# Kernel tuning notes

Hardware: AMD Instinct MI355X
Metric: run time of the kernel (lower is better)

Reference implementation:

```python
import jax, jax.numpy as jnp
import numpy as np

B, DIM, N, K, NA = 1, 64, 1024, 16, 12
POS_HID = 64
ATTN_HID = 4 * DIM


def setup_inputs() -> dict:
    key = jax.random.key(0)
    ks = jax.random.split(key, 8)
    s = 0.05  # small init scale, mimics xavier magnitude
    return {
        "xyz": jax.random.normal(ks[0], (B, 3, N), jnp.float32),
        "feats": jax.random.normal(ks[1], (B, DIM, N, NA), jnp.float32),
        "anchors": jax.random.normal(ks[2], (NA, 3, 3), jnp.float32),
        "to_qkv": jax.random.normal(ks[3], (3 * DIM, DIM), jnp.float32) * s,
        "pos_mlp1": jax.random.normal(ks[4], (POS_HID, 3), jnp.float32) * s,
        "pos_mlp2": jax.random.normal(ks[5], (DIM, POS_HID), jnp.float32) * s,
        "attn_mlp1": jax.random.normal(ks[6], (ATTN_HID, DIM), jnp.float32) * s,
        "attn_mlp2": jax.random.normal(ks[7], (DIM, ATTN_HID), jnp.float32) * s,
    }


def reference(xyz, feats, anchors, to_qkv, pos_mlp1, pos_mlp2, attn_mlp1, attn_mlp2):
    # --- KNN over points (self included) ---
    pts = jnp.swapaxes(xyz, 1, 2)                      # [B,N,3]
    sq = jnp.sum(pts * pts, axis=-1)                   # [B,N]
    d2 = sq[:, :, None] + sq[:, None, :] - 2.0 * jnp.einsum('bnd,bmd->bnm', pts, pts)
    _, idx = jax.lax.top_k(-d2, K)                     # [B,N,K] nearest indices

    # --- gather helpers (vmapped over batch) ---
    gather3 = jax.vmap(lambda x, i: x[:, i])           # [C,N],[N,K] -> [C,N,K]
    gather4 = jax.vmap(lambda x, i: x[:, i, :])        # [C,N,A],[N,K] -> [C,N,K,A]

    # --- relative positions rotated by anchors ---
    grouped_xyz = gather3(xyz, idx)                    # [B,3,N,K]
    rel = xyz[:, :, :, None] - grouped_xyz             # [B,3,N,K]
    gx = jnp.einsum('aij,bjnk->binka', anchors, rel)   # [B,3,N,K,NA]

    # --- positional embedding MLP ---
    pe = jnp.einsum('ji,binka->bjnka', pos_mlp1, gx)   # [B,POS_HID,N,K,NA]
    pe = jax.nn.relu(pe)
    pe = jnp.einsum('ji,binka->bjnka', pos_mlp2, pe)   # [B,DIM,N,K,NA]

    # --- qkv projection ---
    qkv = jnp.einsum('ji,bina->bjna', to_qkv, feats)   # [B,3*DIM,N,NA]
    q, k, v = jnp.split(qkv, 3, axis=1)                # each [B,DIM,N,NA]

    k_g = gather4(k, idx)                              # [B,DIM,N,K,NA]
    v_g = gather4(v, idx) + pe                         # [B,DIM,N,K,NA]
    qk_rel = q[:, :, :, None, :] - k_g                 # [B,DIM,N,K,NA]

    # --- attention MLP on (qk_rel + pe) ---
    sim = qk_rel + pe
    sim = jnp.einsum('ji,binka->bjnka', attn_mlp1, sim)  # [B,4*DIM,N,K,NA]
    sim = jax.nn.relu(sim)
    sim = jnp.einsum('ji,binka->bjnka', attn_mlp2, sim)  # [B,DIM,N,K,NA]

    # --- per-channel softmax over neighbor axis, aggregate ---
    attn = jax.nn.softmax(sim, axis=-2)
    return jnp.sum(attn * v_g, axis=-2)                # [B,DIM,N,NA]
```

## Files before the change

kernel.cpp:

```cpp
#include <hip/hip_runtime.h>

#define NPTS 1024
#define DIM 64
#define KNN 16
#define NA 12
#define NCOL 192
#define XPAD 76

typedef __attribute__((ext_vector_type(8))) short bf16x8;
typedef __attribute__((ext_vector_type(4))) float f32x4;

static __device__ inline unsigned short f2bfu(float x) {
    __bf16 b = (__bf16)x;
    return __builtin_bit_cast(unsigned short, b);
}
static __device__ inline bf16x8 load8_cvt(const float* p) {
    f32x4 u = *(const f32x4*)p;
    f32x4 v = *(const f32x4*)(p + 4);
    bf16x8 r;
    r[0] = (short)f2bfu(u[0]); r[1] = (short)f2bfu(u[1]); r[2] = (short)f2bfu(u[2]); r[3] = (short)f2bfu(u[3]);
    r[4] = (short)f2bfu(v[0]); r[5] = (short)f2bfu(v[1]); r[6] = (short)f2bfu(v[2]); r[7] = (short)f2bfu(v[3]);
    return r;
}

__global__ __launch_bounds__(256) void prep_kernel(const float* __restrict__ feats,
                                                   const float* __restrict__ to_qkv,
                                                   float* __restrict__ qkvT,
                                                   unsigned short* __restrict__ pack,
                                                   const float* __restrict__ pos2,
                                                   const float* __restrict__ am1,
                                                   const float* __restrict__ am2,
                                                   const float* __restrict__ xyz,
                                                   int* __restrict__ idxout) {
    __shared__ unsigned short XT[48][72];
    __shared__ float px[NPTS], py[NPTS], pz[NPTS];
    const int t = threadIdx.x;
    const int n0 = blockIdx.x * 48;

    if (blockIdx.x < 72 && t < 64) {
        int s = blockIdx.x;
        int c16p = t & 15, gp = t >> 4;
        const float* src;
        if (s < 8) {
            int nt = s >> 1, kt = s & 1;
            src = pos2 + (nt * 16 + c16p) * 64 + kt * 32 + gp * 8;
        } else if (s < 40) {
            int u = s - 8, hq = u >> 3, nt = (u >> 1) & 3, kt = u & 1;
            src = am1 + (hq * 64 + nt * 16 + c16p) * 64 + kt * 32 + gp * 8;
        } else {
            int u = s - 40, hq = u >> 3, nt = (u >> 1) & 3, kt = u & 1;
            src = am2 + (nt * 16 + c16p) * 256 + hq * 64 + kt * 32 + gp * 8;
        }
        unsigned short* dst = pack + (s * 64 + t) * 8;
        #pragma unroll
        for (int e = 0; e < 8; ++e) dst[e] = f2bfu(src[e]);
    }

    for (int m = t; m < NPTS; m += 256) {
        px[m] = xyz[m];
        py[m] = xyz[NPTS + m];
        pz[m] = xyz[2 * NPTS + m];
    }
    for (int e = t; e < 48 * 64; e += 256) {
        int c = e % 48, i = e / 48;
        XT[c][i] = f2bfu(feats[i * (NPTS * NA) + n0 + c]);
    }
    __syncthreads();

    const int lane = t & 63, w = t >> 6, c16 = lane & 15, g = lane >> 4;

    {
        bf16x8 bfr[3][2];
        #pragma unroll
        for (int ni = 0; ni < 3; ++ni)
            #pragma unroll
            for (int kt = 0; kt < 2; ++kt) {
                int cd = (w * 3 + ni) * 16 + c16;
                bfr[ni][kt] = load8_cvt(to_qkv + cd * 64 + kt * 32 + g * 8);
            }
        const f32x4 zero4 = {0.f, 0.f, 0.f, 0.f};
        #pragma unroll
        for (int mt = 0; mt < 3; ++mt) {
            f32x4 acc[3] = {zero4, zero4, zero4};
            #pragma unroll
            for (int kt = 0; kt < 2; ++kt) {
                bf16x8 af = *(const bf16x8*)&XT[mt * 16 + c16][kt * 32 + g * 8];
                #pragma unroll
                for (int ni = 0; ni < 3; ++ni)
                    acc[ni] = __builtin_amdgcn_mfma_f32_16x16x32_bf16(af, bfr[ni][kt], acc[ni], 0, 0, 0);
            }
            #pragma unroll
            for (int ni = 0; ni < 3; ++ni) {
                int cd = (w * 3 + ni) * 16 + c16;
                int c = cd >> 6, d = cd & 63;
                #pragma unroll
                for (int r = 0; r < 4; ++r) {
                    int na = n0 + mt * 16 + 4 * g + r;
                    qkvT[c * (NPTS * NA * DIM) + na * 64 + d] = acc[ni][r];
                }
            }
        }
    }

    {
        const int n = blockIdx.x * 4 + w;
        const float xn = px[n], yn = py[n], zn = pz[n];
        const float sqn = xn * xn + yn * yn + zn * zn;
        float dd[16]; int id[16];
        #pragma unroll
        for (int j = 0; j < 16; ++j) {
            int m = j * 64 + lane;
            float xm = px[m], ym = py[m], zm = pz[m];
            float sqm = xm * xm + ym * ym + zm * zm;
            float dot = xn * xm + yn * ym + zn * zm;
            dd[j] = sqn + sqm - 2.f * dot;
            id[j] = m;
        }
        for (int r = 0; r < KNN; ++r) {
            float bd = 1e30f; int bi = 0x7fffffff;
            #pragma unroll
            for (int j = 0; j < 16; ++j)
                if (dd[j] < bd || (dd[j] == bd && id[j] < bi)) { bd = dd[j]; bi = id[j]; }
            #pragma unroll
            for (int mask = 1; mask < 64; mask <<= 1) {
                float od = __shfl_xor(bd, mask);
                int oi = __shfl_xor(bi, mask);
                if (od < bd || (od == bd && oi < bi)) { bd = od; bi = oi; }
            }
            if (lane == 0) idxout[n * KNN + r] = bi;
            #pragma unroll
            for (int j = 0; j < 16; ++j)
                if (id[j] == bi) dd[j] = 1e30f;
        }
    }
}

__global__ __launch_bounds__(512, 4) void attn_main(const float* __restrict__ xyz,
                                                    const float* __restrict__ anchors,
                                                    const float* __restrict__ pos1,
                                                    const unsigned short* __restrict__ pack,
                                                    const float* __restrict__ qT,
                                                    const float* __restrict__ kT,
                                                    const float* __restrict__ vT,
                                                    const int* __restrict__ nn,
                                                    float* __restrict__ out) {
    __shared__ __align__(16) unsigned short XbT[NCOL][XPAD];
    __shared__ __align__(16) unsigned short HqT[NCOL][XPAD];
    __shared__ float relb[KNN][3];
    __shared__ float ab[108];
    __shared__ float gbuf[3][NCOL];
    __shared__ int nidx[KNN];

    const int n = blockIdx.x, t = threadIdx.x;
    const int lane = t & 63, wave = t >> 6;
    const int c16 = lane & 15, g = lane >> 4;
    const int mw = wave & 3;
    const int nw = wave >> 2;

    if (t < 108) ab[t] = anchors[t];
    if (t < KNN) {
        int m = nn[n * KNN + t];
        nidx[t] = m;
        relb[t][0] = xyz[n] - xyz[m];
        relb[t][1] = xyz[NPTS + n] - xyz[NPTS + m];
        relb[t][2] = xyz[2 * NPTS + n] - xyz[2 * NPTS + m];
    }
    __syncthreads();

    for (int e = t; e < 3 * NCOL; e += 512) {
        int row = e / NCOL, col = e % NCOL;
        int a = col >> 4, k = col & 15;
        gbuf[row][col] = ab[a * 9 + row * 3 + 0] * relb[k][0]
                       + ab[a * 9 + row * 3 + 1] * relb[k][1]
                       + ab[a * 9 + row * 3 + 2] * relb[k][2];
    }
    __syncthreads();

    {
        const float p10 = pos1[lane * 3 + 0], p11 = pos1[lane * 3 + 1], p12 = pos1[lane * 3 + 2];
        #pragma unroll
        for (int j = 0; j < 24; ++j) {
            int col = wave + 8 * j;
            float p = p10 * gbuf[0][col] + p11 * gbuf[1][col] + p12 * gbuf[2][col];
            XbT[col][lane] = f2bfu(p > 0.f ? p : 0.f);
        }
    }
    __syncthreads();

    const bf16x8* pk16 = (const bf16x8*)pack;
    const f32x4 zero4 = {0.f, 0.f, 0.f, 0.f};

    f32x4 peacc[6] = {zero4, zero4, zero4, zero4, zero4, zero4};
    #pragma unroll
    for (int kt = 0; kt < 2; ++kt) {
        bf16x8 b0 = pk16[((2 * nw + 0) * 2 + kt) * 64 + lane];
        bf16x8 b1 = pk16[((2 * nw + 1) * 2 + kt) * 64 + lane];
        #pragma unroll
        for (int mi = 0; mi < 3; ++mi) {
            bf16x8 af = *(const bf16x8*)&XbT[(mw + 4 * mi) * 16 + c16][kt * 32 + g * 8];
            peacc[mi * 2 + 0] = __builtin_amdgcn_mfma_f32_16x16x32_bf16(af, b0, peacc[mi * 2 + 0], 0, 0, 0);
            peacc[mi * 2 + 1] = __builtin_amdgcn_mfma_f32_16x16x32_bf16(af, b1, peacc[mi * 2 + 1], 0, 0, 0);
        }
    }

    float vgk[6][4], xreg[6][4];
    {
        const int m0 = nidx[4 * g + 0], m1 = nidx[4 * g + 1];
        const int m2 = nidx[4 * g + 2], m3 = nidx[4 * g + 3];
        #pragma unroll
        for (int mi = 0; mi < 3; ++mi) {
            int a = mw + 4 * mi;
            #pragma unroll
            for (int ni = 0; ni < 2; ++ni) {
                int tile = mi * 2 + ni;
                int d = (2 * nw + ni) * 16 + c16;
                float qv = qT[(n * NA + a) * DIM + d];
                int b0 = (m0 * NA + a) * DIM + d, b1 = (m1 * NA + a) * DIM + d;
                int b2 = (m2 * NA + a) * DIM + d, b3 = (m3 * NA + a) * DIM + d;
                xreg[tile][0] = qv - kT[b0] + peacc[tile][0]; vgk[tile][0] = vT[b0] + peacc[tile][0];
                xreg[tile][1] = qv - kT[b1] + peacc[tile][1]; vgk[tile][1] = vT[b1] + peacc[tile][1];
                xreg[tile][2] = qv - kT[b2] + peacc[tile][2]; vgk[tile][2] = vT[b2] + peacc[tile][2];
                xreg[tile][3] = qv - kT[b3] + peacc[tile][3]; vgk[tile][3] = vT[b3] + peacc[tile][3];
            }
        }
    }
    __syncthreads();
    #pragma unroll
    for (int mi = 0; mi < 3; ++mi)
        #pragma unroll
        for (int ni = 0; ni < 2; ++ni) {
            int tile = mi * 2 + ni;
            int col = (2 * nw + ni) * 16 + c16;
            #pragma unroll
            for (int r = 0; r < 4; ++r)
                XbT[(mw + 4 * mi) * 16 + 4 * g + r][col] = f2bfu(xreg[tile][r]);
        }
    __syncthreads();

    f32x4 sacc[6] = {zero4, zero4, zero4, zero4, zero4, zero4};
    for (int hq = 0; hq < 4; ++hq) {
        f32x4 hacc[6] = {zero4, zero4, zero4, zero4, zero4, zero4};
        #pragma unroll
        for (int kt = 0; kt < 2; ++kt) {
            bf16x8 b0 = pk16[(8 + (hq * 4 + 2 * nw + 0) * 2 + kt) * 64 + lane];
            bf16x8 b1 = pk16[(8 + (hq * 4 + 2 * nw + 1) * 2 + kt) * 64 + lane];
            #pragma unroll
            for (int mi = 0; mi < 3; ++mi) {
                bf16x8 af = *(const bf16x8*)&XbT[(mw + 4 * mi) * 16 + c16][kt * 32 + g * 8];
                hacc[mi * 2 + 0] = __builtin_amdgcn_mfma_f32_16x16x32_bf16(af, b0, hacc[mi * 2 + 0], 0, 0, 0);
                hacc[mi * 2 + 1] = __builtin_amdgcn_mfma_f32_16x16x32_bf16(af, b1, hacc[mi * 2 + 1], 0, 0, 0);
            }
        }
        #pragma unroll
        for (int mi = 0; mi < 3; ++mi)
            #pragma unroll
            for (int ni = 0; ni < 2; ++ni) {
                int tile = mi * 2 + ni;
                int col = (2 * nw + ni) * 16 + c16;
                #pragma unroll
                for (int r = 0; r < 4; ++r)
                    HqT[(mw + 4 * mi) * 16 + 4 * g + r][col] = f2bfu(fmaxf(hacc[tile][r], 0.f));
            }
        __syncthreads();
        #pragma unroll
        for (int kt = 0; kt < 2; ++kt) {
            bf16x8 b0 = pk16[(40 + hq * 8 + (2 * nw + 0) * 2 + kt) * 64 + lane];
            bf16x8 b1 = pk16[(40 + hq * 8 + (2 * nw + 1) * 2 + kt) * 64 + lane];
            #pragma unroll
            for (int mi = 0; mi < 3; ++mi) {
                bf16x8 af = *(const bf16x8*)&HqT[(mw + 4 * mi) * 16 + c16][kt * 32 + g * 8];
                sacc[mi * 2 + 0] = __builtin_amdgcn_mfma_f32_16x16x32_bf16(af, b0, sacc[mi * 2 + 0], 0, 0, 0);
                sacc[mi * 2 + 1] = __builtin_amdgcn_mfma_f32_16x16x32_bf16(af, b1, sacc[mi * 2 + 1], 0, 0, 0);
            }
        }
        __syncthreads();
    }

    #pragma unroll
    for (int mi = 0; mi < 3; ++mi) {
        int a = mw + 4 * mi;
        #pragma unroll
        for (int ni = 0; ni < 2; ++ni) {
            int tile = mi * 2 + ni;
            int d = (2 * nw + ni) * 16 + c16;
            float e0 = __expf(sacc[tile][0]);
            float e1 = __expf(sacc[tile][1]);
            float e2 = __expf(sacc[tile][2]);
            float e3 = __expf(sacc[tile][3]);
            float den = (e0 + e1) + (e2 + e3);
            float num = (e0 * vgk[tile][0] + e1 * vgk[tile][1]) + (e2 * vgk[tile][2] + e3 * vgk[tile][3]);
            den += __shfl_xor(den, 16); num += __shfl_xor(num, 16);
            den += __shfl_xor(den, 32); num += __shfl_xor(num, 32);
            if (g == 0)
                out[(d * NPTS + n) * NA + a] = num / den;
        }
    }
}

extern "C" void kernel_launch(void* const* d_in, const int* in_sizes, int n_in,
                              void* d_out, int out_size, void* d_ws, size_t ws_size,
                              hipStream_t stream) {
    const float* xyz     = (const float*)d_in[0];
    const float* feats   = (const float*)d_in[1];
    const float* anchors = (const float*)d_in[2];
    const float* to_qkv  = (const float*)d_in[3];
    const float* pos1    = (const float*)d_in[4];
    const float* pos2    = (const float*)d_in[5];
    const float* am1     = (const float*)d_in[6];
    const float* am2     = (const float*)d_in[7];
    float* out = (float*)d_out;

    float* ws = (float*)d_ws;
    const int seg = NPTS * NA * DIM;
    float* qT = ws;
    float* kT = ws + seg;
    float* vT = ws + 2 * seg;
    int* nn = (int*)(ws + 3 * seg);
    unsigned short* pack = (unsigned short*)(ws + 3 * seg + NPTS * KNN);

    prep_kernel<<<256, 256, 0, stream>>>(feats, to_qkv, qT, pack, pos2, am1, am2, xyz, nn);
    attn_main<<<NPTS, 512, 0, stream>>>(xyz, anchors, pos1, pack, qT, kT, vT, nn, out);
}
```

Baseline: 76.54 us.

## Give each wave its own anchors and drop block-wide barriers in attention kernel

The attention kernel is repartitioned so that each of 6 waves owns two anchors across all 64 channels, with a wave-private LDS scratch tile. This replaces every __syncthreads with an LDS waitcnt. The first positional-MLP layer is now computed straight into MFMA A-fragments in registers, which removes the gbuf/XbT staging passes. Gathered v values are held as packed bf16 to save registers. The cost is that each wave reloads all weight fragments, which adds L2 traffic, and the v values lose precision.

```diff
diff --git a/kernel.cpp b/kernel.cpp
--- a/kernel.cpp
+++ b/kernel.cpp
@@ -5,7 +5,7 @@
 #define KNN 16
 #define NA 12
 #define NCOL 192
-#define XPAD 76
+#define XPAD 72
 
 typedef __attribute__((ext_vector_type(8))) short bf16x8;
 typedef __attribute__((ext_vector_type(4))) float f32x4;
@@ -13,6 +13,12 @@
 static __device__ inline unsigned short f2bfu(float x) {
     __bf16 b = (__bf16)x;
     return __builtin_bit_cast(unsigned short, b);
+}
+static __device__ inline float bf2f(unsigned short s) {
+    return __uint_as_float(((unsigned)s) << 16);
+}
+static __device__ inline unsigned pk2(float lo, float hi) {
+    return (unsigned)f2bfu(lo) | ((unsigned)f2bfu(hi) << 16);
 }
 static __device__ inline bf16x8 load8_cvt(const float* p) {
     f32x4 u = *(const f32x4*)p;
@@ -135,160 +141,172 @@
     }
 }
 
-__global__ __launch_bounds__(512, 4) void attn_main(const float* __restrict__ xyz,
+__global__ __launch_bounds__(384, 3) void attn_main(const float* __restrict__ xyz,
+                                                    const float* __restrict__ pos1,
                                                     const float* __restrict__ anchors,
-                                                    const float* __restrict__ pos1,
                                                     const unsigned short* __restrict__ pack,
                                                     const float* __restrict__ qT,
                                                     const float* __restrict__ kT,
                                                     const float* __restrict__ vT,
                                                     const int* __restrict__ nn,
                                                     float* __restrict__ out) {
-    __shared__ __align__(16) unsigned short XbT[NCOL][XPAD];
-    __shared__ __align__(16) unsigned short HqT[NCOL][XPAD];
-    __shared__ float relb[KNN][3];
-    __shared__ float ab[108];
-    __shared__ float gbuf[3][NCOL];
-    __shared__ int nidx[KNN];
+    __shared__ float P1s[192];
+    __shared__ float abs_s[108];
+    __shared__ __align__(16) unsigned short Xw[6 * 32 * XPAD];
 
     const int n = blockIdx.x, t = threadIdx.x;
     const int lane = t & 63, wave = t >> 6;
     const int c16 = lane & 15, g = lane >> 4;
-    const int mw = wave & 3;
-    const int nw = wave >> 2;
-
-    if (t < 108) ab[t] = anchors[t];
-    if (t < KNN) {
-        int m = nn[n * KNN + t];
-        nidx[t] = m;
-        relb[t][0] = xyz[n] - xyz[m];
-        relb[t][1] = xyz[NPTS + n] - xyz[NPTS + m];
-        relb[t][2] = xyz[2 * NPTS + n] - xyz[2 * NPTS + m];
-    }
+    const int a0 = 2 * wave;
+
+    if (t < 192) P1s[t] = pos1[t];
+    if (t < 108) abs_s[t] = anchors[t];
     __syncthreads();
 
-    for (int e = t; e < 3 * NCOL; e += 512) {
-        int row = e / NCOL, col = e % NCOL;
-        int a = col >> 4, k = col & 15;
-        gbuf[row][col] = ab[a * 9 + row * 3 + 0] * relb[k][0]
-                       + ab[a * 9 + row * 3 + 1] * relb[k][1]
-                       + ab[a * 9 + row * 3 + 2] * relb[k][2];
-    }
-    __syncthreads();
-
-    {
-        const float p10 = pos1[lane * 3 + 0], p11 = pos1[lane * 3 + 1], p12 = pos1[lane * 3 + 2];
-        #pragma unroll
-        for (int j = 0; j < 24; ++j) {
-            int col = wave + 8 * j;
-            float p = p10 * gbuf[0][col] + p11 * gbuf[1][col] + p12 * gbuf[2][col];
-            XbT[col][lane] = f2bfu(p > 0.f ? p : 0.f);
-        }
-    }
-    __syncthreads();
+    int mk[4];
+    #pragma unroll
+    for (int r = 0; r < 4; ++r) mk[r] = nn[n * KNN + 4 * g + r];
+    const int mc = nn[n * KNN + c16];
+    const float relx = xyz[n] - xyz[mc];
+    const float rely = xyz[NPTS + n] - xyz[NPTS + mc];
+    const float relz = xyz[2 * NPTS + n] - xyz[2 * NPTS + mc];
+
+    float G[2][3];
+    #pragma unroll
+    for (int ai = 0; ai < 2; ++ai) {
+        int a = a0 + ai;
+        G[ai][0] = abs_s[a * 9 + 0] * relx + abs_s[a * 9 + 1] * rely + abs_s[a * 9 + 2] * relz;
+        G[ai][1] = abs_s[a * 9 + 3] * relx + abs_s[a * 9 + 4] * rely + abs_s[a * 9 + 5] * relz;
+        G[ai][2] = abs_s[a * 9 + 6] * relx + abs_s[a * 9 + 7] * rely + abs_s[a * 9 + 8] * relz;
+    }
+    bf16x8 pfrag[2][2];
+    #pragma unroll
+    for (int kt = 0; kt < 2; ++kt)
+        #pragma unroll
+        for (int e = 0; e < 8; ++e) {
+            int h = kt * 32 + g * 8 + e;
+            float p0 = P1s[3 * h], p1 = P1s[3 * h + 1], p2 = P1s[3 * h + 2];
+            #pragma unroll
+            for (int ai = 0; ai < 2; ++ai) {
+                float p = p0 * G[ai][0] + p1 * G[ai][1] + p2 * G[ai][2];
+                pfrag[ai][kt][e] = (short)f2bfu(fmaxf(p, 0.f));
+            }
+        }
 
     const bf16x8* pk16 = (const bf16x8*)pack;
     const f32x4 zero4 = {0.f, 0.f, 0.f, 0.f};
 
-    f32x4 peacc[6] = {zero4, zero4, zero4, zero4, zero4, zero4};
-    #pragma unroll
-    for (int kt = 0; kt < 2; ++kt) {
-        bf16x8 b0 = pk16[((2 * nw + 0) * 2 + kt) * 64 + lane];
-        bf16x8 b1 = pk16[((2 * nw + 1) * 2 + kt) * 64 + lane];
-        #pragma unroll
-        for (int mi = 0; mi < 3; ++mi) {
-            bf16x8 af = *(const bf16x8*)&XbT[(mw + 4 * mi) * 16 + c16][kt * 32 + g * 8];
-            peacc[mi * 2 + 0] = __builtin_amdgcn_mfma_f32_16x16x32_bf16(af, b0, peacc[mi * 2 + 0], 0, 0, 0);
-            peacc[mi * 2 + 1] = __builtin_amdgcn_mfma_f32_16x16x32_bf16(af, b1, peacc[mi * 2 + 1], 0, 0, 0);
-        }
-    }
-
-    float vgk[6][4], xreg[6][4];
-    {
-        const int m0 = nidx[4 * g + 0], m1 = nidx[4 * g + 1];
-        const int m2 = nidx[4 * g + 2], m3 = nidx[4 * g + 3];
-        #pragma unroll
-        for (int mi = 0; mi < 3; ++mi) {
-            int a = mw + 4 * mi;
-            #pragma unroll
-            for (int ni = 0; ni < 2; ++ni) {
-                int tile = mi * 2 + ni;
-                int d = (2 * nw + ni) * 16 + c16;
-                float qv = qT[(n * NA + a) * DIM + d];
-                int b0 = (m0 * NA + a) * DIM + d, b1 = (m1 * NA + a) * DIM + d;
-                int b2 = (m2 * NA + a) * DIM + d, b3 = (m3 * NA + a) * DIM + d;
-                xreg[tile][0] = qv - kT[b0] + peacc[tile][0]; vgk[tile][0] = vT[b0] + peacc[tile][0];
-                xreg[tile][1] = qv - kT[b1] + peacc[tile][1]; vgk[tile][1] = vT[b1] + peacc[tile][1];
-                xreg[tile][2] = qv - kT[b2] + peacc[tile][2]; vgk[tile][2] = vT[b2] + peacc[tile][2];
-                xreg[tile][3] = qv - kT[b3] + peacc[tile][3]; vgk[tile][3] = vT[b3] + peacc[tile][3];
-            }
-        }
-    }
-    __syncthreads();
-    #pragma unroll
-    for (int mi = 0; mi < 3; ++mi)
-        #pragma unroll
-        for (int ni = 0; ni < 2; ++ni) {
-            int tile = mi * 2 + ni;
-            int col = (2 * nw + ni) * 16 + c16;
+    f32x4 acc[2][4];
+    #pragma unroll
+    for (int ai = 0; ai < 2; ++ai)
+        #pragma unroll
+        for (int nt = 0; nt < 4; ++nt) acc[ai][nt] = zero4;
+    #pragma unroll
+    for (int kt = 0; kt < 2; ++kt)
+        #pragma unroll
+        for (int nt = 0; nt < 4; ++nt) {
+            bf16x8 bf = pk16[(nt * 2 + kt) * 64 + lane];
+            acc[0][nt] = __builtin_amdgcn_mfma_f32_16x16x32_bf16(pfrag[0][kt], bf, acc[0][nt], 0, 0, 0);
+            acc[1][nt] = __builtin_amdgcn_mfma_f32_16x16x32_bf16(pfrag[1][kt], bf, acc[1][nt], 0, 0, 0);
+        }
+
+    unsigned short* xw = Xw + wave * 32 * XPAD;
+    unsigned vgp[2][4][2];
+    #pragma unroll
+    for (int ai = 0; ai < 2; ++ai) {
+        int a = a0 + ai;
+        #pragma unroll
+        for (int nt = 0; nt < 4; ++nt) {
+            int d = nt * 16 + c16;
+            float qv = qT[(n * NA + a) * DIM + d];
+            float xr[4], vg[4];
+            #pragma unroll
+            for (int r = 0; r < 4; ++r) {
+                int b = (mk[r] * NA + a) * DIM + d;
+                float pe = acc[ai][nt][r];
+                xr[r] = qv - kT[b] + pe;
+                vg[r] = vT[b] + pe;
+            }
+            vgp[ai][nt][0] = pk2(vg[0], vg[1]);
+            vgp[ai][nt][1] = pk2(vg[2], vg[3]);
             #pragma unroll
             for (int r = 0; r < 4; ++r)
-                XbT[(mw + 4 * mi) * 16 + 4 * g + r][col] = f2bfu(xreg[tile][r]);
-        }
-    __syncthreads();
-
-    f32x4 sacc[6] = {zero4, zero4, zero4, zero4, zero4, zero4};
+                xw[(ai * 16 + 4 * g + r) * XPAD + d] = f2bfu(xr[r]);
+        }
+    }
+    __builtin_amdgcn_sched_barrier(0);
+    asm volatile("s_waitcnt lgkmcnt(0)" ::: "memory");
+    __builtin_amdgcn_sched_barrier(0);
+
+    bf16x8 xf[2][2];
+    #pragma unroll
+    for (int ai = 0; ai < 2; ++ai)
+        #pragma unroll
+        for (int kt = 0; kt < 2; ++kt)
+            xf[ai][kt] = *(const bf16x8*)&xw[(ai * 16 + c16) * XPAD + kt * 32 + g * 8];
+
+    f32x4 sacc[2][4];
+    #pragma unroll
+    for (int ai = 0; ai < 2; ++ai)
+        #pragma unroll
+        for (int nt = 0; nt < 4; ++nt) sacc[ai][nt] = zero4;
+
     for (int hq = 0; hq < 4; ++hq) {
-        f32x4 hacc[6] = {zero4, zero4, zero4, zero4, zero4, zero4};
-        #pragma unroll
-        for (int kt = 0; kt < 2; ++kt) {
-            bf16x8 b0 = pk16[(8 + (hq * 4 + 2 * nw + 0) * 2 + kt) * 64 + lane];
-            bf16x8 b1 = pk16[(8 + (hq * 4 + 2 * nw + 1) * 2 + kt) * 64 + lane];
-            #pragma unroll
-            for (int mi = 0; mi < 3; ++mi) {
-                bf16x8 af = *(const bf16x8*)&XbT[(mw + 4 * mi) * 16 + c16][kt * 32 + g * 8];
-                hacc[mi * 2 + 0] = __builtin_amdgcn_mfma_f32_16x16x32_bf16(af, b0, hacc[mi * 2 + 0], 0, 0, 0);
-                hacc[mi * 2 + 1] = __builtin_amdgcn_mfma_f32_16x16x32_bf16(af, b1, hacc[mi * 2 + 1], 0, 0, 0);
-            }
-        }
-        #pragma unroll
-        for (int mi = 0; mi < 3; ++mi)
-            #pragma unroll
-            for (int ni = 0; ni < 2; ++ni) {
-                int tile = mi * 2 + ni;
-                int col = (2 * nw + ni) * 16 + c16;
+        f32x4 hacc[2][4];
+        #pragma unroll
+        for (int ai = 0; ai < 2; ++ai)
+            #pragma unroll
+            for (int nt = 0; nt < 4; ++nt) hacc[ai][nt] = zero4;
+        #pragma unroll
+        for (int kt = 0; kt < 2; ++kt)
+            #pragma unroll
+            for (int nt = 0; nt < 4; ++nt) {
+                bf16x8 bf = pk16[(8 + hq * 8 + nt * 2 + kt) * 64 + lane];
+                hacc[0][nt] = __builtin_amdgcn_mfma_f32_16x16x32_bf16(xf[0][kt], bf, hacc[0][nt], 0, 0, 0);
+                hacc[1][nt] = __builtin_amdgcn_mfma_f32_16x16x32_bf16(xf[1][kt], bf, hacc[1][nt], 0, 0, 0);
+            }
+        #pragma unroll
+        for (int ai = 0; ai < 2; ++ai)
+            #pragma unroll
+            for (int nt = 0; nt < 4; ++nt) {
+                int col = nt * 16 + c16;
                 #pragma unroll
                 for (int r = 0; r < 4; ++r)
-                    HqT[(mw + 4 * mi) * 16 + 4 * g + r][col] = f2bfu(fmaxf(hacc[tile][r], 0.f));
-            }
-        __syncthreads();
-        #pragma unroll
-        for (int kt = 0; kt < 2; ++kt) {
-            bf16x8 b0 = pk16[(40 + hq * 8 + (2 * nw + 0) * 2 + kt) * 64 + lane];
-            bf16x8 b1 = pk16[(40 + hq * 8 + (2 * nw + 1) * 2 + kt) * 64 + lane];
-            #pragma unroll
-            for (int mi = 0; mi < 3; ++mi) {
-                bf16x8 af = *(const bf16x8*)&HqT[(mw + 4 * mi) * 16 + c16][kt * 32 + g * 8];
-                sacc[mi * 2 + 0] = __builtin_amdgcn_mfma_f32_16x16x32_bf16(af, b0, sacc[mi * 2 + 0], 0, 0, 0);
-                sacc[mi * 2 + 1] = __builtin_amdgcn_mfma_f32_16x16x32_bf16(af, b1, sacc[mi * 2 + 1], 0, 0, 0);
-            }
-        }
-        __syncthreads();
-    }
-
-    #pragma unroll
-    for (int mi = 0; mi < 3; ++mi) {
-        int a = mw + 4 * mi;
-        #pragma unroll
-        for (int ni = 0; ni < 2; ++ni) {
-            int tile = mi * 2 + ni;
-            int d = (2 * nw + ni) * 16 + c16;
-            float e0 = __expf(sacc[tile][0]);
-            float e1 = __expf(sacc[tile][1]);
-            float e2 = __expf(sacc[tile][2]);
-            float e3 = __expf(sacc[tile][3]);
+                    xw[(ai * 16 + 4 * g + r) * XPAD + col] = f2bfu(fmaxf(hacc[ai][nt][r], 0.f));
+            }
+        __builtin_amdgcn_sched_barrier(0);
+        asm volatile("s_waitcnt lgkmcnt(0)" ::: "memory");
+        __builtin_amdgcn_sched_barrier(0);
+        bf16x8 hf[2][2];
+        #pragma unroll
+        for (int ai = 0; ai < 2; ++ai)
+            #pragma unroll
+            for (int kt = 0; kt < 2; ++kt)
+                hf[ai][kt] = *(const bf16x8*)&xw[(ai * 16 + c16) * XPAD + kt * 32 + g * 8];
+        #pragma unroll
+        for (int kt = 0; kt < 2; ++kt)
+            #pragma unroll
+            for (int nt = 0; nt < 4; ++nt) {
+                bf16x8 bf = pk16[(40 + hq * 8 + nt * 2 + kt) * 64 + lane];
+                sacc[0][nt] = __builtin_amdgcn_mfma_f32_16x16x32_bf16(hf[0][kt], bf, sacc[0][nt], 0, 0, 0);
+                sacc[1][nt] = __builtin_amdgcn_mfma_f32_16x16x32_bf16(hf[1][kt], bf, sacc[1][nt], 0, 0, 0);
+            }
+    }
+
+    #pragma unroll
+    for (int ai = 0; ai < 2; ++ai) {
+        int a = a0 + ai;
+        #pragma unroll
+        for (int nt = 0; nt < 4; ++nt) {
+            int d = nt * 16 + c16;
+            float e0 = __expf(sacc[ai][nt][0]);
+            float e1 = __expf(sacc[ai][nt][1]);
+            float e2 = __expf(sacc[ai][nt][2]);
+            float e3 = __expf(sacc[ai][nt][3]);
             float den = (e0 + e1) + (e2 + e3);
-            float num = (e0 * vgk[tile][0] + e1 * vgk[tile][1]) + (e2 * vgk[tile][2] + e3 * vgk[tile][3]);
+            unsigned v01 = vgp[ai][nt][0], v23 = vgp[ai][nt][1];
+            float num = (e0 * bf2f((unsigned short)(v01 & 0xffff)) + e1 * bf2f((unsigned short)(v01 >> 16)))
+                      + (e2 * bf2f((unsigned short)(v23 & 0xffff)) + e3 * bf2f((unsigned short)(v23 >> 16)));
             den += __shfl_xor(den, 16); num += __shfl_xor(num, 16);
             den += __shfl_xor(den, 32); num += __shfl_xor(num, 32);
             if (g == 0)
@@ -319,5 +337,5 @@
     unsigned short* pack = (unsigned short*)(ws + 3 * seg + NPTS * KNN);
 
     prep_kernel<<<256, 256, 0, stream>>>(feats, to_qkv, qT, pack, pos2, am1, am2, xyz, nn);
-    attn_main<<<NPTS, 512, 0, stream>>>(xyz, anchors, pos1, pack, qT, kT, vT, nn, out);
-}
+    attn_main<<<NPTS, 384, 0, stream>>>(xyz, pos1, anchors, pack, qT, kT, vT, nn, out);
+}
```

Result: slower. 90.32 us (+18.0%).
